# Kernel tuning notes

Measured on AMD Instinct MI355X. Metric: run time of the kernel, lower is better.

Reference implementation:

```python
import jax, jax.numpy as jnp
import numpy as np

B, TENC, EPROJS, DUNITS, ODIM, L, ATT_DIM = 64, 800, 512, 512, 5000, 128, 320
SOS = EOS = ODIM - 1


def setup_inputs() -> dict:
    key = jax.random.key(0)
    ks = jax.random.split(key, 16)
    s = 0.02
    D = DUNITS
    return {
        "hpad": jax.random.normal(ks[0], (B, TENC, EPROJS), jnp.float32),
        # keep lengths in [TENC//2, TENC] so every row has valid frames
        "hlen": jnp.clip(jax.random.randint(ks[1], (B,), 0, TENC + 1), TENC // 2, TENC).astype(jnp.int32),
        "ys": jax.random.randint(ks[2], (B, L), 0, ODIM - 1),  # int labels (exclude eos)
        "embed": s * jax.random.normal(ks[3], (ODIM, D), jnp.float32),
        # torch.nn.LSTMCell params: gates order (i, f, g, o)
        "W_ih0": s * jax.random.normal(ks[4], (4 * D, D + EPROJS), jnp.float32),
        "W_hh0": s * jax.random.normal(ks[5], (4 * D, D), jnp.float32),
        "b_ih0": jnp.zeros((4 * D,), jnp.float32),
        "b_hh0": jnp.zeros((4 * D,), jnp.float32),
        "W_ih1": s * jax.random.normal(ks[6], (4 * D, D), jnp.float32),
        "W_hh1": s * jax.random.normal(ks[7], (4 * D, D), jnp.float32),
        "b_ih1": jnp.zeros((4 * D,), jnp.float32),
        "b_hh1": jnp.zeros((4 * D,), jnp.float32),
        # AttDot attention projections (no bias, as in espnet mlp_enc/mlp_dec usage)
        "Wa_enc": s * jax.random.normal(ks[8], (EPROJS, ATT_DIM), jnp.float32),
        "Wa_dec": s * jax.random.normal(ks[9], (D, ATT_DIM), jnp.float32),
        "W_out": s * jax.random.normal(ks[10], (ODIM, D), jnp.float32),
        "b_out": jnp.zeros((ODIM,), jnp.float32),
    }


def _lstm_cell(x, h, c, Wi, Wh, bi, bh):
    g = x @ Wi.T + bi + h @ Wh.T + bh
    i, f, gg, o = jnp.split(g, 4, axis=-1)
    c2 = jax.nn.sigmoid(f) * c + jax.nn.sigmoid(i) * jnp.tanh(gg)
    h2 = jax.nn.sigmoid(o) * jnp.tanh(c2)
    return h2, c2


def _forward(hpad, hlen, ys, embed, W_ih0, W_hh0, b_ih0, b_hh0,
             W_ih1, W_hh1, b_ih1, b_hh1, Wa_enc, Wa_dec, W_out, b_out):
    D = DUNITS
    tmask = jnp.arange(TENC)[None, :] < hlen[:, None]          # [B, T]
    hm = hpad * tmask[:, :, None]                               # mask_by_length
    enc_pre = jnp.tanh(jnp.einsum('bte,ea->bta', hm, Wa_enc))   # [B, T, A] precomputed

    sos_col = jnp.full((B, 1), SOS, ys.dtype)
    eos_col = jnp.full((B, 1), EOS, ys.dtype)
    ys_in = jnp.concatenate([sos_col, ys], axis=1)              # [B, L+1]
    ys_out = jnp.concatenate([ys, eos_col], axis=1)             # [B, L+1]
    eys = embed[ys_in]                                          # [B, L+1, D]

    zeros = jnp.zeros((B, D), hpad.dtype)
    carry0 = (zeros, zeros, zeros, zeros)  # z0, c0, z1, c1

    def step(carry, ey_t):
        z0, c0, z1, c1 = carry
        # AttDot: e = <tanh(enc W), tanh(z0 W)> with length masking
        d = jnp.tanh(z0 @ Wa_dec)                               # [B, A]
        e = jnp.einsum('ba,bta->bt', d, enc_pre)                # [B, T]
        e = jnp.where(tmask, e, jnp.float32(-1e9))
        w = jax.nn.softmax(e, axis=-1)
        att_c = jnp.einsum('bt,bte->be', w, hm)                 # [B, eprojs]
        x = jnp.concatenate([ey_t, att_c], axis=-1)             # [B, D+eprojs]
        z0, c0 = _lstm_cell(x, z0, c0, W_ih0, W_hh0, b_ih0, b_hh0)
        z1, c1 = _lstm_cell(z0, z1, c1, W_ih1, W_hh1, b_ih1, b_hh1)
        return (z0, c0, z1, c1), z1                             # gen_feat='s' -> top hidden

    _, z_all = jax.lax.scan(step, carry0, jnp.swapaxes(eys, 0, 1))  # [L+1, B, D]
    z_all = jnp.swapaxes(z_all, 0, 1)                           # [B, L+1, D]

    logits = jnp.einsum('bld,vd->blv', z_all, W_out) + b_out    # [B, L+1, V]
    logp = jax.nn.log_softmax(logits, axis=-1)
    nll = -jnp.take_along_axis(logp, ys_out[..., None], axis=-1)[..., 0]
    # F.cross_entropy mean over all tokens (no padding here), then *= mean(len(ys_in)) - 1 = L
    loss = nll.mean() * jnp.float32(L)
    acc = (logits.argmax(-1) == ys_out).mean()
    return loss, acc


def reference(hpad, hlen, ys, embed, W_ih0, W_hh0, b_ih0, b_hh0,
              W_ih1, W_hh1, b_ih1, b_hh1, Wa_enc, Wa_dec, W_out, b_out):
    return _forward(hpad, hlen, ys, embed, W_ih0, W_hh0, b_ih0, b_hh0,
                    W_ih1, W_hh1, b_ih1, b_hh1, Wa_enc, Wa_dec, W_out, b_out)
```

## Files before the change

### kernel.cpp

```cpp
#include <hip/hip_runtime.h>
#include <math.h>

typedef unsigned short u16;
typedef float f32x4 __attribute__((ext_vector_type(4)));
typedef short s16x8 __attribute__((ext_vector_type(8)));

#define ODIM 5000
#define NROWS 8256

__device__ inline u16 f2bf(float f){
  unsigned u = __float_as_uint(f);
  return (u16)((u + 0x7FFFu + ((u >> 16) & 1u)) >> 16);
}
__device__ inline float bf2f(u16 h){ return __uint_as_float(((unsigned)h) << 16); }
__device__ inline float sigm(float x){ return 1.f/(1.f + expf(-x)); }

__global__ void a0_init(float* att2, float* dz, float* z0f, float* z1f,
                        float* c0, float* c1, float* accum){
  int tid = blockIdx.x*256 + threadIdx.x, n = 64*256;
  for (int i=tid;i<2*64*516;i+=n) att2[i]=0.f;
  for (int i=tid;i<10240;i+=n) dz[i]=0.f;
  for (int i=tid;i<32768;i+=n){ z0f[i]=0.f; z1f[i]=0.f; c0[i]=0.f; c1[i]=0.f; }
  if (tid < 8) accum[tid]=0.f;
}

__global__ void a1_wcvt(const float* waenc, const float* wadec,
  const float* wih0, const float* whh0, const float* wih1, const float* whh1,
  const float* bih0, const float* bhh0, const float* bih1, const float* bhh1,
  const float* wout,
  u16* waencT, u16* wadecT, u16* wcat0, u16* wcat1, u16* wee, u16* woutb,
  float* bc0, float* bc1)
{
  int tid = blockIdx.x*blockDim.x + threadIdx.x;
  int nth = gridDim.x*blockDim.x;
  for (int i=tid; i<320*512; i+=nth){
    int n=i>>9, k=i&511;
    waencT[i] = f2bf(waenc[k*320+n]);
    wadecT[i] = f2bf(wadec[k*320+n]);
  }
  for (int i=tid; i<2048*1024; i+=nth){
    int np=i>>10, k=i&1023;
    int u=np>>2, g=np&3, r=g*512+u;
    wcat0[i] = f2bf(k<512 ? wih0[r*1024+512+k] : whh0[r*512+(k-512)]);
    wcat1[i] = f2bf(k<512 ? wih1[r*512+k]      : whh1[r*512+(k-512)]);
  }
  for (int i=tid; i<2048*512; i+=nth){
    int np=i>>9, k=i&511;
    int u=np>>2, g=np&3, r=g*512+u;
    wee[i] = f2bf(wih0[r*1024+k]);
  }
  for (int i=tid; i<5000*512; i+=nth) woutb[i] = f2bf(wout[i]);
  for (int i=tid; i<2048; i+=nth){
    int u=i>>2, g=i&3, r=g*512+u;
    bc0[i] = bih0[r]+bhh0[r];
    bc1[i] = bih1[r]+bhh1[r];
  }
}

__global__ __launch_bounds__(256) void a2_encpre(
  const float* __restrict__ hpad, const int* __restrict__ hlen,
  const u16* __restrict__ waencT, u16* __restrict__ hm, u16* __restrict__ encp)
{
  __shared__ u16 A[64][40];
  __shared__ u16 BT[320][40];
  int tid = threadIdx.x, blk = blockIdx.x;
  int wave = tid>>6, lane = tid&63;
  f32x4 acc[20];
  #pragma unroll
  for (int f=0;f<20;f++) acc[f] = (f32x4){0.f,0.f,0.f,0.f};
  int srow = tid>>2, skoff = (tid&3)*8;
  int grow_s = blk*64 + srow;
  int b_s = grow_s/800, t_s = grow_s - b_s*800;
  bool valid_s = t_s < hlen[b_s];
  for (int c=0;c<16;c++){
    int k0 = c*32;
    {
      const float* src = hpad + (size_t)grow_s*512 + k0 + skoff;
      float4 v0 = *(const float4*)(src);
      float4 v1 = *(const float4*)(src+4);
      if (!valid_s){ v0 = make_float4(0,0,0,0); v1 = make_float4(0,0,0,0); }
      short4 p0 = make_short4((short)f2bf(v0.x),(short)f2bf(v0.y),(short)f2bf(v0.z),(short)f2bf(v0.w));
      short4 p1 = make_short4((short)f2bf(v1.x),(short)f2bf(v1.y),(short)f2bf(v1.z),(short)f2bf(v1.w));
      *(short4*)&A[srow][skoff]   = p0;
      *(short4*)&A[srow][skoff+4] = p1;
      *(short4*)(hm + (size_t)grow_s*512 + k0 + skoff)     = p0;
      *(short4*)(hm + (size_t)grow_s*512 + k0 + skoff + 4) = p1;
    }
    for (int id=tid; id<1280; id+=256){
      int n = id>>2, kv = (id&3)*8;
      *(s16x8*)&BT[n][kv] = *(const s16x8*)(waencT + n*512 + k0 + kv);
    }
    __syncthreads();
    s16x8 av = *(const s16x8*)&A[wave*16 + (lane&15)][(lane>>4)*8];
    #pragma unroll
    for (int f=0;f<20;f++){
      s16x8 bv = *(const s16x8*)&BT[f*16+(lane&15)][(lane>>4)*8];
      acc[f] = __builtin_amdgcn_mfma_f32_16x16x32_bf16(av,bv,acc[f],0,0,0);
    }
    __syncthreads();
  }
  #pragma unroll
  for (int f=0;f<20;f++){
    int col = f*16 + (lane&15);
    #pragma unroll
    for (int r=0;r<4;r++){
      int grow = blk*64 + wave*16 + (lane>>4)*4 + r;
      encp[(size_t)grow*320 + col] = f2bf(tanhf(acc[f][r]));
    }
  }
}

__global__ __launch_bounds__(256) void a3_geys(
  const int* __restrict__ ys, const float* __restrict__ embed,
  const u16* __restrict__ wee, const float* __restrict__ bc0,
  u16* __restrict__ geys)
{
  __shared__ u16 A[64][88];
  __shared__ u16 BT[256][88];
  int t = blockIdx.x, nt = blockIdx.y, tid = threadIdx.x;
  int wave=tid>>6, lane=tid&63;
  f32x4 acc[16];
  #pragma unroll
  for (int f=0;f<16;f++) acc[f]=(f32x4){0.f,0.f,0.f,0.f};
  int srow = tid>>2, skoff=(tid&3)*16;
  int idx = (t==0) ? (ODIM-1) : ys[srow*128 + (t-1)];
  const float* asrc = embed + (size_t)idx*512;
  for (int c=0;c<8;c++){
    int k0=c*64;
    #pragma unroll
    for (int i=0;i<16;i+=4){
      float4 v = *(const float4*)(asrc + k0 + skoff + i);
      *(short4*)&A[srow][skoff+i] =
        make_short4((short)f2bf(v.x),(short)f2bf(v.y),(short)f2bf(v.z),(short)f2bf(v.w));
    }
    for (int id=tid; id<2048; id+=256){
      int n = id>>3, kv=(id&7)*8;
      *(s16x8*)&BT[n][kv] = *(const s16x8*)(wee + (size_t)(nt*256+n)*512 + k0 + kv);
    }
    __syncthreads();
    #pragma unroll
    for (int kk=0;kk<64;kk+=32){
      s16x8 av = *(const s16x8*)&A[wave*16+(lane&15)][kk+(lane>>4)*8];
      #pragma unroll
      for (int f=0;f<16;f++){
        s16x8 bv = *(const s16x8*)&BT[f*16+(lane&15)][kk+(lane>>4)*8];
        acc[f] = __builtin_amdgcn_mfma_f32_16x16x32_bf16(av,bv,acc[f],0,0,0);
      }
    }
    __syncthreads();
  }
  #pragma unroll
  for (int f=0;f<16;f++){
    int colL = f*16+(lane&15);
    int gc = nt*256+colL;
    float bb = bc0[gc];
    #pragma unroll
    for (int r=0;r<4;r++){
      int row = wave*16 + (lane>>4)*4 + r;
      geys[(size_t)(t*64+row)*2048 + gc] = f2bf(acc[f][r] + bb);
    }
  }
}

__global__ __launch_bounds__(256) void k1_att(
  const u16* __restrict__ d_g, const u16* __restrict__ encp,
  const u16* __restrict__ hm, const int* __restrict__ hlen,
  float* __restrict__ att)
{
  int b = blockIdx.x >> 3, ch = blockIdx.x & 7;
  int wave = threadIdx.x >> 6, lane = threadIdx.x & 63;
  int len = hlen[b];
  float dreg[8];
  {
    s16x8 dv = 0;
    if (lane < 40) dv = *(const s16x8*)(d_g + b*320 + lane*8);
    #pragma unroll
    for (int j=0;j<8;j++) dreg[j] = bf2f((u16)dv[j]);
  }
  float attacc[8];
  #pragma unroll
  for (int j=0;j<8;j++) attacc[j]=0.f;
  float sacc = 0.f;
  int t0 = ch*100;
  int tend = t0+100 < len ? t0+100 : len;
  for (int i0 = t0 + wave; i0 < tend; i0 += 16){
    s16x8 ev[4], hv[4];
    #pragma unroll
    for (int q=0;q<4;q++){
      int tt = i0 + 4*q;
      if (tt < tend){
        if (lane<40) ev[q] = *(const s16x8*)(encp + (size_t)(b*800+tt)*320 + lane*8);
        hv[q] = *(const s16x8*)(hm + (size_t)(b*800+tt)*512 + lane*8);
      }
    }
    #pragma unroll
    for (int q=0;q<4;q++){
      int tt = i0 + 4*q;
      if (tt < tend){
        float e = 0.f;
        if (lane<40){
          #pragma unroll
          for (int j=0;j<8;j++) e += dreg[j]*bf2f((u16)ev[q][j]);
        }
        #pragma unroll
        for (int off=32; off; off>>=1) e += __shfl_xor(e, off);
        float pw = expf(fminf(e, 60.f));
        sacc += pw;
        #pragma unroll
        for (int j=0;j<8;j++) attacc[j] += pw*bf2f((u16)hv[q][j]);
      }
    }
  }
  __shared__ float attl[4][512];
  __shared__ float sl[4];
  #pragma unroll
  for (int j=0;j<8;j++) attl[wave][lane*8+j] = attacc[j];
  if (lane==0) sl[wave] = sacc;
  __syncthreads();
  for (int c = threadIdx.x; c < 512; c += 256){
    float v = attl[0][c]+attl[1][c]+attl[2][c]+attl[3][c];
    atomicAdd(&att[b*516 + c], v);
  }
  if (threadIdx.x==0) atomicAdd(&att[b*516 + 512], sl[0]+sl[1]+sl[2]+sl[3]);
}

__global__ __launch_bounds__(256) void k2_cell0(
  const float* __restrict__ attp, float* __restrict__ attz,
  const u16* __restrict__ z0p, u16* __restrict__ z0n,
  float* __restrict__ c0,
  const u16* __restrict__ wcat0, const u16* __restrict__ geyt)
{
  __shared__ __align__(16) char smem[16896];
  __shared__ float sinv[64];
  u16 (*A)[88]  = (u16(*)[88])smem;
  u16 (*BT)[88] = (u16(*)[88])(smem+11264);
  int tid = threadIdx.x, nb = blockIdx.x;
  int wave=tid>>6, lane=tid&63;
  if (tid < 64) sinv[tid] = 1.f/attp[tid*516+512];
  __syncthreads();
  f32x4 acc[2];
  acc[0]=(f32x4){0.f,0.f,0.f,0.f}; acc[1]=(f32x4){0.f,0.f,0.f,0.f};
  int srow=tid>>2, skoff=(tid&3)*16;
  int brow=tid>>3, bkoff=(tid&7)*8;
  for (int c=0;c<16;c++){
    int k0=c*64;
    if (c<8){
      const float* src = attp + srow*516 + k0 + skoff;
      float sv = sinv[srow];
      #pragma unroll
      for (int i=0;i<16;i+=4){
        float4 v = *(const float4*)(src+i);
        *(short4*)&A[srow][skoff+i] = make_short4(
          (short)f2bf(v.x*sv),(short)f2bf(v.y*sv),(short)f2bf(v.z*sv),(short)f2bf(v.w*sv));
      }
    } else {
      const u16* src = z0p + srow*512 + (k0-512) + skoff;
      *(s16x8*)&A[srow][skoff]   = *(const s16x8*)(src);
      *(s16x8*)&A[srow][skoff+8] = *(const s16x8*)(src+8);
    }
    *(s16x8*)&BT[brow][bkoff] = *(const s16x8*)(wcat0 + (size_t)(nb*32+brow)*1024 + k0 + bkoff);
    __syncthreads();
    #pragma unroll
    for (int kk=0;kk<64;kk+=32){
      s16x8 av = *(const s16x8*)&A[wave*16+(lane&15)][kk+(lane>>4)*8];
      #pragma unroll
      for (int f=0;f<2;f++){
        s16x8 bv = *(const s16x8*)&BT[f*16+(lane&15)][kk+(lane>>4)*8];
        acc[f] = __builtin_amdgcn_mfma_f32_16x16x32_bf16(av,bv,acc[f],0,0,0);
      }
    }
    __syncthreads();
  }
  float (*gl)[36] = (float(*)[36])smem;
  #pragma unroll
  for (int f=0;f<2;f++){
    int colL = f*16+(lane&15);
    #pragma unroll
    for (int r=0;r<4;r++){
      int rowL = wave*16+(lane>>4)*4+r;
      gl[rowL][colL] = acc[f][r] + bf2f(geyt[rowL*2048 + nb*32 + colL]);
    }
  }
  __syncthreads();
  for (int it=tid; it<512; it+=256){
    int bb=it>>3, ul=it&7;
    float gi=gl[bb][ul*4], gf=gl[bb][ul*4+1], gg=gl[bb][ul*4+2], go=gl[bb][ul*4+3];
    int ug = nb*8+ul;
    float cp = c0[bb*512+ug];
    float cn = sigm(gf)*cp + sigm(gi)*tanhf(gg);
    float z = sigm(go)*tanhf(cn);
    c0[bb*512+ug]=cn;
    z0n[bb*512+ug]=f2bf(z);
  }
  for (int i=tid + nb*256; i < 64*516; i += 64*256) attz[i] = 0.f;
}

__global__ __launch_bounds__(256) void k3_cell1(
  const u16* __restrict__ z0n, const u16* __restrict__ z1p,
  u16* __restrict__ z1n, float* __restrict__ c1,
  const u16* __restrict__ wcat1, const float* __restrict__ bc1,
  u16* __restrict__ zallt,
  const u16* __restrict__ wadecT, u16* __restrict__ d_g)
{
  __shared__ __align__(16) char smem[25600];
  int tid = threadIdx.x, wave=tid>>6, lane=tid&63;
  int blk = blockIdx.x;
  u16 (*A)[88]  = (u16(*)[88])smem;
  if (blk < 64){
    u16 (*BT)[88] = (u16(*)[88])(smem+11264);
    int nb = blk;
    f32x4 acc[2];
    acc[0]=(f32x4){0.f,0.f,0.f,0.f}; acc[1]=(f32x4){0.f,0.f,0.f,0.f};
    int srow=tid>>2, skoff=(tid&3)*16;
    int brow=tid>>3, bkoff=(tid&7)*8;
    for (int c=0;c<16;c++){
      int k0=c*64;
      const u16* asrc = (c<8) ? (z0n + srow*512 + k0 + skoff)
                              : (z1p + srow*512 + (k0-512) + skoff);
      *(s16x8*)&A[srow][skoff]   = *(const s16x8*)asrc;
      *(s16x8*)&A[srow][skoff+8] = *(const s16x8*)(asrc+8);
      *(s16x8*)&BT[brow][bkoff] = *(const s16x8*)(wcat1 + (size_t)(nb*32+brow)*1024 + k0 + bkoff);
      __syncthreads();
      #pragma unroll
      for (int kk=0;kk<64;kk+=32){
        s16x8 av = *(const s16x8*)&A[wave*16+(lane&15)][kk+(lane>>4)*8];
        #pragma unroll
        for (int f=0;f<2;f++){
          s16x8 bv = *(const s16x8*)&BT[f*16+(lane&15)][kk+(lane>>4)*8];
          acc[f] = __builtin_amdgcn_mfma_f32_16x16x32_bf16(av,bv,acc[f],0,0,0);
        }
      }
      __syncthreads();
    }
    float (*gl)[36] = (float(*)[36])smem;
    #pragma unroll
    for (int f=0;f<2;f++){
      int colL = f*16+(lane&15);
      float bb = bc1[nb*32+colL];
      #pragma unroll
      for (int r=0;r<4;r++){
        int rowL = wave*16+(lane>>4)*4+r;
        gl[rowL][colL] = acc[f][r] + bb;
      }
    }
    __syncthreads();
    for (int it=tid; it<512; it+=256){
      int bb=it>>3, ul=it&7;
      float gi=gl[bb][ul*4], gf=gl[bb][ul*4+1], gg=gl[bb][ul*4+2], go=gl[bb][ul*4+3];
      int ug = nb*8+ul;
      float cp = c1[bb*512+ug];
      float cn = sigm(gf)*cp + sigm(gi)*tanhf(gg);
      float z = sigm(go)*tanhf(cn);
      c1[bb*512+ug]=cn;
      u16 zb = f2bf(z);
      z1n[bb*512+ug]=zb;
      zallt[bb*512+ug]=zb;
    }
  } else {
    u16 (*BT)[88] = (u16(*)[88])(smem+11264);
    int nb = blk-64;
    f32x4 acc[5];
    #pragma unroll
    for (int f=0;f<5;f++) acc[f]=(f32x4){0.f,0.f,0.f,0.f};
    int srow=tid>>2, skoff=(tid&3)*16;
    for (int c=0;c<8;c++){
      int k0=c*64;
      const u16* asrc = z0n + srow*512 + k0 + skoff;
      *(s16x8*)&A[srow][skoff]   = *(const s16x8*)asrc;
      *(s16x8*)&A[srow][skoff+8] = *(const s16x8*)(asrc+8);
      for (int id=tid; id<640; id+=256){
        int n=id>>3, kv=(id&7)*8;
        *(s16x8*)&BT[n][kv] = *(const s16x8*)(wadecT + (size_t)(nb*80+n)*512 + k0 + kv);
      }
      __syncthreads();
      #pragma unroll
      for (int kk=0;kk<64;kk+=32){
        s16x8 av = *(const s16x8*)&A[wave*16+(lane&15)][kk+(lane>>4)*8];
        #pragma unroll
        for (int f=0;f<5;f++){
          s16x8 bv = *(const s16x8*)&BT[f*16+(lane&15)][kk+(lane>>4)*8];
          acc[f] = __builtin_amdgcn_mfma_f32_16x16x32_bf16(av,bv,acc[f],0,0,0);
        }
      }
      __syncthreads();
    }
    #pragma unroll
    for (int f=0;f<5;f++){
      int col = nb*80 + f*16 + (lane&15);
      #pragma unroll
      for (int r=0;r<4;r++){
        int row = wave*16 + (lane>>4)*4 + r;
        d_g[row*320+col] = f2bf(tanhf(acc[f][r]));
      }
    }
  }
}

__global__ __launch_bounds__(512) void k4_logits(
  const u16* __restrict__ zall, const u16* __restrict__ woutb,
  const float* __restrict__ b_out, const int* __restrict__ ys,
  float* __restrict__ partials)
{
  __shared__ char smem[46080];
  u16 (*A)[40]  = (u16(*)[40])smem;
  u16 (*BT)[40] = (u16(*)[40])(smem + 5120);
  int t = blockIdx.x, v = blockIdx.y;
  int tid = threadIdx.x, wave = tid>>6, lane = tid&63;
  int mf = wave>>1;
  int nh = (wave&1)*256;
  f32x4 acc[16];
  #pragma unroll
  for (int f=0;f<16;f++) acc[f]=(f32x4){0.f,0.f,0.f,0.f};
  for (int c=0;c<16;c++){
    int k0 = c*32;
    { int row = tid>>3, koff=(tid&7)*4;
      *(short4*)&A[row][koff] = *(const short4*)(zall + (size_t)(t*64+row)*512 + k0 + koff); }
    { int n = v*512 + tid;
      if (n < ODIM){
        const u16* src = woutb + (size_t)n*512 + k0;
        #pragma unroll
        for (int i=0;i<32;i+=8) *(s16x8*)&BT[tid][i] = *(const s16x8*)(src+i);
      } else {
        s16x8 z = 0;
        #pragma unroll
        for (int i=0;i<32;i+=8) *(s16x8*)&BT[tid][i] = z;
      }
    }
    __syncthreads();
    s16x8 av = *(const s16x8*)&A[mf*16 + (lane&15)][(lane>>4)*8];
    #pragma unroll
    for (int f=0;f<16;f++){
      s16x8 bv = *(const s16x8*)&BT[nh + f*16 + (lane&15)][(lane>>4)*8];
      acc[f] = __builtin_amdgcn_mfma_f32_16x16x32_bf16(av,bv,acc[f],0,0,0);
    }
    __syncthreads();
  }
  float (*ll)[512] = (float(*)[512])smem;
  for (int g=0; g<4; g++){
    if (mf == g){
      #pragma unroll
      for (int f=0;f<16;f++){
        int colL = nh + f*16 + (lane&15);
        int gcol = v*512 + colL;
        float bo = (gcol < ODIM) ? b_out[gcol] : 0.f;
        #pragma unroll
        for (int r=0;r<4;r++){
          int rowL = (lane>>4)*4 + r;
          ll[rowL][colL] = acc[f][r] + bo;
        }
      }
    }
    __syncthreads();
    int r = tid>>5, j = tid&31;
    float m = -1e30f, s = 0.f, amax = -1e30f; int aidx = 0;
    #pragma unroll
    for (int i=0;i<16;i++){
      int cL = j + 32*i;
      int gc = v*512 + cL;
      if (gc < ODIM){
        float val = ll[r][cL];
        if (val > m){ s = s*expf(m-val) + 1.f; m = val; }
        else s += expf(val - m);
        if (val > amax){ amax = val; aidx = gc; }
      }
    }
    #pragma unroll
    for (int off=16; off; off>>=1){
      float mo = __shfl_xor(m, off), so = __shfl_xor(s, off);
      float ao = __shfl_xor(amax, off); int io = __shfl_xor(aidx, off);
      float M = fmaxf(m, mo);
      s = s*expf(m-M) + so*expf(mo-M);
      m = M;
      if (ao > amax || (ao == amax && io < aidx)){ amax = ao; aidx = io; }
    }
    if (j == 0){
      int b = g*16 + r;
      int grow = t*64 + b;
      int lab = (t < 128) ? ys[b*128 + t] : (ODIM-1);
      float labval = 0.f, labf = 0.f;
      int lo = lab - v*512;
      if (lo >= 0 && lo < 512){ labval = ll[r][lo]; labf = 1.f; }
      float* pp = partials + (size_t)(grow*10 + v)*8;
      pp[0]=m; pp[1]=s; pp[2]=amax; pp[3]=__int_as_float(aidx); pp[4]=labval; pp[5]=labf;
    }
    __syncthreads();
  }
}

__global__ __launch_bounds__(256) void k5_loss(
  const float* __restrict__ partials, const int* __restrict__ ys, float* accum)
{
  int row = blockIdx.x*256 + threadIdx.x;
  float nll = 0.f; int corr = 0;
  if (row < NROWS){
    float M=-1e30f, S=0.f, amax=-1e30f, labval=0.f; int aidx=0;
    for (int v=0;v<10;v++){
      const float* pp = partials + (size_t)(row*10+v)*8;
      float m=pp[0], s=pp[1], a=pp[2]; int ai=__float_as_int(pp[3]);
      float MM = fmaxf(M, m);
      S = S*expf(M-MM) + s*expf(m-MM);
      M = MM;
      if (a > amax || (a == amax && ai < aidx)){ amax=a; aidx=ai; }
      if (pp[5] != 0.f) labval = pp[4];
    }
    nll = M + logf(S) - labval;
    int t = row>>6, b = row&63;
    int lab = (t < 128) ? ys[b*128+t] : (ODIM-1);
    corr = (aidx == lab) ? 1 : 0;
  }
  __shared__ float sn[256]; __shared__ int sc[256];
  sn[threadIdx.x]=nll; sc[threadIdx.x]=corr; __syncthreads();
  for (int st=128; st; st>>=1){
    if (threadIdx.x<st){ sn[threadIdx.x]+=sn[threadIdx.x+st]; sc[threadIdx.x]+=sc[threadIdx.x+st]; }
    __syncthreads();
  }
  if (threadIdx.x==0){
    atomicAdd(accum, sn[0]);
    atomicAdd((int*)accum + 1, sc[0]);
  }
}

__global__ void k6_final(const float* accum, float* out){
  out[0] = accum[0]/(float)NROWS * 128.f;
  out[1] = (float)(((const int*)accum)[1])/(float)NROWS;
}

extern "C" void kernel_launch(void* const* d_in, const int* in_sizes, int n_in,
                              void* d_out, int out_size, void* d_ws, size_t ws_size,
                              hipStream_t stream)
{
  const float* hpad  = (const float*)d_in[0];
  const int*   hlen  = (const int*)d_in[1];
  const int*   ys    = (const int*)d_in[2];
  const float* embed = (const float*)d_in[3];
  const float* wih0  = (const float*)d_in[4];
  const float* whh0  = (const float*)d_in[5];
  const float* bih0  = (const float*)d_in[6];
  const float* bhh0  = (const float*)d_in[7];
  const float* wih1  = (const float*)d_in[8];
  const float* whh1  = (const float*)d_in[9];
  const float* bih1  = (const float*)d_in[10];
  const float* bhh1  = (const float*)d_in[11];
  const float* waenc = (const float*)d_in[12];
  const float* wadec = (const float*)d_in[13];
  const float* wout  = (const float*)d_in[14];
  const float* bout  = (const float*)d_in[15];

  char* ws = (char*)d_ws;
  u16*   hm      = (u16*)(ws + 0);
  u16*   encp    = (u16*)(ws + 52428800);
  u16*   waencT  = (u16*)(ws + 85196800);
  u16*   wadecT  = (u16*)(ws + 85524480);
  u16*   wcat0   = (u16*)(ws + 85852160);
  u16*   wcat1   = (u16*)(ws + 90046464);
  u16*   wee     = (u16*)(ws + 94240768);
  u16*   woutb   = (u16*)(ws + 96337920);
  float* bc0     = (float*)(ws + 101457920);
  float* bc1     = (float*)(ws + 101466112);
  u16*   geys    = (u16*)(ws + 101474304);
  u16*   d_g     = (u16*)(ws + 135290880);
  float* att     = (float*)(ws + 135331840);
  u16*   z0b     = (u16*)(ws + 135596032);
  u16*   z1b     = (u16*)(ws + 135727104);
  float* c0      = (float*)(ws + 135858176);
  float* c1      = (float*)(ws + 135989248);
  u16*   zall    = (u16*)(ws + 136120320);
  float* partials= (float*)(ws + 144574464);
  float* accum   = (float*)(ws + 147216384);

  a0_init<<<64,256,0,stream>>>(att, (float*)d_g, (float*)z0b, (float*)z1b, c0, c1, accum);
  a1_wcvt<<<512,256,0,stream>>>(waenc, wadec, wih0, whh0, wih1, whh1,
                                bih0, bhh0, bih1, bhh1, wout,
                                waencT, wadecT, wcat0, wcat1, wee, woutb, bc0, bc1);
  a2_encpre<<<800,256,0,stream>>>(hpad, hlen, waencT, hm, encp);
  a3_geys<<<dim3(129,8),256,0,stream>>>(ys, embed, wee, bc0, geys);

  for (int t=0; t<129; t++){
    int p = t & 1;
    k1_att<<<512,256,0,stream>>>(d_g, encp, hm, hlen, att + p*64*516);
    k2_cell0<<<64,256,0,stream>>>(att + p*64*516, att + (p^1)*64*516,
                                  z0b + (p^1)*64*512, z0b + p*64*512,
                                  c0, wcat0, geys + (size_t)t*64*2048);
    k3_cell1<<<68,256,0,stream>>>(z0b + p*64*512, z1b + (p^1)*64*512,
                                  z1b + p*64*512, c1, wcat1, bc1,
                                  zall + (size_t)t*64*512, wadecT, d_g);
  }

  k4_logits<<<dim3(129,10),512,0,stream>>>(zall, woutb, bout, ys, partials);
  k5_loss<<<33,256,0,stream>>>(partials, ys, accum);
  k6_final<<<1,1,0,stream>>>(accum, (float*)d_out);
}
```

Baseline: 6.811 ms.

## Store masked encoder states and attention keys in FP8 to halve attention traffic

```diff
diff --git a/kernel.cpp b/kernel.cpp
--- a/kernel.cpp
+++ b/kernel.cpp
@@ -2,6 +2,7 @@
 #include <math.h>
 
 typedef unsigned short u16;
+typedef unsigned char u8;
 typedef float f32x4 __attribute__((ext_vector_type(4)));
 typedef short s16x8 __attribute__((ext_vector_type(8)));
 
@@ -14,6 +15,26 @@
 }
 __device__ inline float bf2f(u16 h){ return __uint_as_float(((unsigned)h) << 16); }
 __device__ inline float sigm(float x){ return 1.f/(1.f + expf(-x)); }
+
+__device__ inline unsigned f2fp8(float f){
+  unsigned u = __float_as_uint(f);
+  unsigned s = (u>>24)&0x80u;
+  int e = (int)((u>>23)&0xffu) - 127;
+  if (e < -7) return s;
+  unsigned full = (u & 0x7fffffu) | 0x800000u;
+  unsigned keep = full >> 20;
+  unsigned rem  = full & 0xFFFFFu;
+  keep += (rem > 0x80000u) || (rem == 0x80000u && (keep & 1u));
+  int te = e + 7;
+  if (keep >= 16u){ keep >>= 1; te += 1; }
+  if (te >= 16) return s | 0x7Eu;
+  if (te < 1)  return s;
+  return s | ((unsigned)te<<3) | (keep & 7u);
+}
+__device__ inline float fp8d(unsigned v){
+  unsigned r = ((v & 0x80u) << 24) | (((v & 0x7fu) + 960u) << 20);
+  return __uint_as_float(r);
+}
 
 __global__ void a0_init(float* att2, float* dz, float* z0f, float* z1f,
                         float* c0, float* c1, float* accum){
@@ -59,7 +80,7 @@
 
 __global__ __launch_bounds__(256) void a2_encpre(
   const float* __restrict__ hpad, const int* __restrict__ hlen,
-  const u16* __restrict__ waencT, u16* __restrict__ hm, u16* __restrict__ encp)
+  const u16* __restrict__ waencT, u8* __restrict__ hm8, u8* __restrict__ encp8)
 {
   __shared__ u16 A[64][40];
   __shared__ u16 BT[320][40];
@@ -79,12 +100,13 @@
       float4 v0 = *(const float4*)(src);
       float4 v1 = *(const float4*)(src+4);
       if (!valid_s){ v0 = make_float4(0,0,0,0); v1 = make_float4(0,0,0,0); }
-      short4 p0 = make_short4((short)f2bf(v0.x),(short)f2bf(v0.y),(short)f2bf(v0.z),(short)f2bf(v0.w));
-      short4 p1 = make_short4((short)f2bf(v1.x),(short)f2bf(v1.y),(short)f2bf(v1.z),(short)f2bf(v1.w));
-      *(short4*)&A[srow][skoff]   = p0;
-      *(short4*)&A[srow][skoff+4] = p1;
-      *(short4*)(hm + (size_t)grow_s*512 + k0 + skoff)     = p0;
-      *(short4*)(hm + (size_t)grow_s*512 + k0 + skoff + 4) = p1;
+      *(short4*)&A[srow][skoff] = make_short4(
+        (short)f2bf(v0.x),(short)f2bf(v0.y),(short)f2bf(v0.z),(short)f2bf(v0.w));
+      *(short4*)&A[srow][skoff+4] = make_short4(
+        (short)f2bf(v1.x),(short)f2bf(v1.y),(short)f2bf(v1.z),(short)f2bf(v1.w));
+      unsigned lo = f2fp8(v0.x) | (f2fp8(v0.y)<<8) | (f2fp8(v0.z)<<16) | (f2fp8(v0.w)<<24);
+      unsigned hi = f2fp8(v1.x) | (f2fp8(v1.y)<<8) | (f2fp8(v1.z)<<16) | (f2fp8(v1.w)<<24);
+      *(uint2*)(hm8 + (size_t)grow_s*512 + k0 + skoff) = make_uint2(lo, hi);
     }
     for (int id=tid; id<1280; id+=256){
       int n = id>>2, kv = (id&3)*8;
@@ -105,7 +127,7 @@
     #pragma unroll
     for (int r=0;r<4;r++){
       int grow = blk*64 + wave*16 + (lane>>4)*4 + r;
-      encp[(size_t)grow*320 + col] = f2bf(tanhf(acc[f][r]));
+      encp8[(size_t)grow*320 + col] = (u8)f2fp8(tanhf(acc[f][r]));
     }
   }
 }
@@ -163,8 +185,8 @@
 }
 
 __global__ __launch_bounds__(256) void k1_att(
-  const u16* __restrict__ d_g, const u16* __restrict__ encp,
-  const u16* __restrict__ hm, const int* __restrict__ hlen,
+  const u16* __restrict__ d_g, const u8* __restrict__ encp8,
+  const u8* __restrict__ hm8, const int* __restrict__ hlen,
   float* __restrict__ att)
 {
   int b = blockIdx.x >> 3, ch = blockIdx.x & 7;
@@ -184,13 +206,13 @@
   int t0 = ch*100;
   int tend = t0+100 < len ? t0+100 : len;
   for (int i0 = t0 + wave; i0 < tend; i0 += 16){
-    s16x8 ev[4], hv[4];
+    uint2 ea[4], ha[4];
     #pragma unroll
     for (int q=0;q<4;q++){
       int tt = i0 + 4*q;
       if (tt < tend){
-        if (lane<40) ev[q] = *(const s16x8*)(encp + (size_t)(b*800+tt)*320 + lane*8);
-        hv[q] = *(const s16x8*)(hm + (size_t)(b*800+tt)*512 + lane*8);
+        if (lane<40) ea[q] = *(const uint2*)(encp8 + (size_t)(b*800+tt)*320 + lane*8);
+        ha[q] = *(const uint2*)(hm8 + (size_t)(b*800+tt)*512 + lane*8);
       }
     }
     #pragma unroll
@@ -199,15 +221,25 @@
       if (tt < tend){
         float e = 0.f;
         if (lane<40){
-          #pragma unroll
-          for (int j=0;j<8;j++) e += dreg[j]*bf2f((u16)ev[q][j]);
+          unsigned w0 = ea[q].x, w1 = ea[q].y;
+          e += dreg[0]*fp8d(w0&0xffu) + dreg[1]*fp8d((w0>>8)&0xffu)
+             + dreg[2]*fp8d((w0>>16)&0xffu) + dreg[3]*fp8d(w0>>24);
+          e += dreg[4]*fp8d(w1&0xffu) + dreg[5]*fp8d((w1>>8)&0xffu)
+             + dreg[6]*fp8d((w1>>16)&0xffu) + dreg[7]*fp8d(w1>>24);
         }
         #pragma unroll
         for (int off=32; off; off>>=1) e += __shfl_xor(e, off);
         float pw = expf(fminf(e, 60.f));
         sacc += pw;
-        #pragma unroll
-        for (int j=0;j<8;j++) attacc[j] += pw*bf2f((u16)hv[q][j]);
+        unsigned h0 = ha[q].x, h1 = ha[q].y;
+        attacc[0] += pw*fp8d(h0&0xffu);
+        attacc[1] += pw*fp8d((h0>>8)&0xffu);
+        attacc[2] += pw*fp8d((h0>>16)&0xffu);
+        attacc[3] += pw*fp8d(h0>>24);
+        attacc[4] += pw*fp8d(h1&0xffu);
+        attacc[5] += pw*fp8d((h1>>8)&0xffu);
+        attacc[6] += pw*fp8d((h1>>16)&0xffu);
+        attacc[7] += pw*fp8d(h1>>24);
       }
     }
   }
@@ -435,7 +467,7 @@
     }
     __syncthreads();
   }
-  float (*ll)[512] = (float(*)[512])smem;
+  float (*ll)[518] = (float(*)[518])smem;
   for (int g=0; g<4; g++){
     if (mf == g){
       #pragma unroll
@@ -547,37 +579,37 @@
   const float* bout  = (const float*)d_in[15];
 
   char* ws = (char*)d_ws;
-  u16*   hm      = (u16*)(ws + 0);
-  u16*   encp    = (u16*)(ws + 52428800);
-  u16*   waencT  = (u16*)(ws + 85196800);
-  u16*   wadecT  = (u16*)(ws + 85524480);
-  u16*   wcat0   = (u16*)(ws + 85852160);
-  u16*   wcat1   = (u16*)(ws + 90046464);
-  u16*   wee     = (u16*)(ws + 94240768);
-  u16*   woutb   = (u16*)(ws + 96337920);
-  float* bc0     = (float*)(ws + 101457920);
-  float* bc1     = (float*)(ws + 101466112);
-  u16*   geys    = (u16*)(ws + 101474304);
-  u16*   d_g     = (u16*)(ws + 135290880);
-  float* att     = (float*)(ws + 135331840);
-  u16*   z0b     = (u16*)(ws + 135596032);
-  u16*   z1b     = (u16*)(ws + 135727104);
-  float* c0      = (float*)(ws + 135858176);
-  float* c1      = (float*)(ws + 135989248);
-  u16*   zall    = (u16*)(ws + 136120320);
-  float* partials= (float*)(ws + 144574464);
-  float* accum   = (float*)(ws + 147216384);
+  u8*    hm8     = (u8*)(ws + 0);
+  u8*    encp8   = (u8*)(ws + 26214400);
+  u16*   waencT  = (u16*)(ws + 42598400);
+  u16*   wadecT  = (u16*)(ws + 42926080);
+  u16*   wcat0   = (u16*)(ws + 43253760);
+  u16*   wcat1   = (u16*)(ws + 47448064);
+  u16*   wee     = (u16*)(ws + 51642368);
+  u16*   woutb   = (u16*)(ws + 53739520);
+  float* bc0     = (float*)(ws + 58859520);
+  float* bc1     = (float*)(ws + 58867712);
+  u16*   geys    = (u16*)(ws + 58875904);
+  u16*   d_g     = (u16*)(ws + 92692480);
+  float* att     = (float*)(ws + 92733440);
+  u16*   z0b     = (u16*)(ws + 92997632);
+  u16*   z1b     = (u16*)(ws + 93128704);
+  float* c0      = (float*)(ws + 93259776);
+  float* c1      = (float*)(ws + 93390848);
+  u16*   zall    = (u16*)(ws + 93521920);
+  float* partials= (float*)(ws + 101976064);
+  float* accum   = (float*)(ws + 104617984);
 
   a0_init<<<64,256,0,stream>>>(att, (float*)d_g, (float*)z0b, (float*)z1b, c0, c1, accum);
   a1_wcvt<<<512,256,0,stream>>>(waenc, wadec, wih0, whh0, wih1, whh1,
                                 bih0, bhh0, bih1, bhh1, wout,
                                 waencT, wadecT, wcat0, wcat1, wee, woutb, bc0, bc1);
-  a2_encpre<<<800,256,0,stream>>>(hpad, hlen, waencT, hm, encp);
+  a2_encpre<<<800,256,0,stream>>>(hpad, hlen, waencT, hm8, encp8);
   a3_geys<<<dim3(129,8),256,0,stream>>>(ys, embed, wee, bc0, geys);
 
   for (int t=0; t<129; t++){
     int p = t & 1;
-    k1_att<<<512,256,0,stream>>>(d_g, encp, hm, hlen, att + p*64*516);
+    k1_att<<<512,256,0,stream>>>(d_g, encp8, hm8, hlen, att + p*64*516);
     k2_cell0<<<64,256,0,stream>>>(att + p*64*516, att + (p^1)*64*516,
                                   z0b + (p^1)*64*512, z0b + p*64*512,
                                   c0, wcat0, geys + (size_t)t*64*2048);
```

After: 7.018 ms. 1.03x slower.
